# Optimization experiments

Hardware: AMD Instinct MI355X
Metric: run time of the kernel (lower is better)

Reference implementation:

```python
import jax, jax.numpy as jnp
import numpy as np

EPS = 1e-8  # matches torch F.cosine_similarity default eps


def setup_inputs() -> dict:
    key = jax.random.key(0)
    k1, k2, k3 = jax.random.split(key, 3)
    B, S, Q, T, D = 1, 5, 512, 64, 2048
    supp = jax.random.normal(k1, (B, S, T, D), dtype=jnp.float32)
    query = jax.random.normal(k2, (B, Q, T, D), dtype=jnp.float32)
    query_ys = jax.random.randint(k3, (Q,), 0, S, dtype=jnp.int64)
    return {"supp": supp, "query": query, "query_ys": query_ys}


def reference(supp, query, query_ys):
    # supp: [B, S, T, D], query: [B, Q, T, D]
    # Pool once over T (mathematically identical to repeat-then-mean).
    sp = supp.mean(axis=-2)   # [B, S, D]
    qp = query.mean(axis=-2)  # [B, Q, D]
    # Pairwise cosine similarity over D -> [B, Q, S]
    num = jnp.einsum('bqd,bsd->bqs', qp, sp)
    qn = jnp.linalg.norm(qp, axis=-1)  # [B, Q]
    sn = jnp.linalg.norm(sp, axis=-1)  # [B, S]
    denom = jnp.maximum(qn[:, :, None] * sn[:, None, :], EPS)
    dist = (num / denom)[0]  # squeeze(0) -> [Q, S]
    # Cross-entropy over the num_supp (class) axis
    logp = jax.nn.log_softmax(dist, axis=-1)
    loss = -jnp.take_along_axis(logp, query_ys[:, None], axis=1).mean()
    return (loss, 1.0 - dist)
```

## Files before the change

### kernel.cpp

```cpp
#include <hip/hip_runtime.h>
#include <hip/hip_bf16.h>

#define S_DIM 5
#define Q_DIM 512
#define T_DIM 64
#define D_DIM 2048
#define EPS_CS 1e-8f

typedef float f32x4 __attribute__((ext_vector_type(4)));

#define WS_SP     0
#define WS_SNPART 10240
#define WS_LOSS   10280
#define WS_CNT    10281

__device__ __forceinline__ float wave_reduce_sum(float v) {
    #pragma unroll
    for (int off = 32; off > 0; off >>= 1)
        v += __shfl_down(v, off, 64);
    return v;
}

__device__ __forceinline__ float dot4(f32x4 a, f32x4 b) {
    return a.x * b.x + a.y * b.y + a.z * b.z + a.w * b.w;
}

__global__ __launch_bounds__(512) void supp_pool_kernel(
    const float* __restrict__ supp, float* __restrict__ sp,
    float* __restrict__ snpart, float* __restrict__ loss_acc,
    unsigned int* __restrict__ counter)
{
    if (blockIdx.x == 0 && threadIdx.x == 0) {
        *loss_acc = 0.0f;
        *counter  = 0u;
    }

    const int s    = blockIdx.x >> 3;
    const int c    = blockIdx.x & 7;
    const int tg   = threadIdx.x >> 6;
    const int lane = threadIdx.x & 63;
    const int slot = c * 64 + lane;

    const f32x4* base = (const f32x4*)(supp + (size_t)s * T_DIM * D_DIM);

    f32x4 acc = {0.f, 0.f, 0.f, 0.f};
    #pragma unroll
    for (int i = 0; i < 8; ++i) {
        const int t = tg * 8 + i;
        acc += base[t * (D_DIM / 4) + slot];
    }

    __shared__ f32x4 lds[8][64];
    lds[tg][lane] = acc;
    __syncthreads();
    if (tg == 0) {
        f32x4 tot = lds[0][lane];
        #pragma unroll
        for (int w = 1; w < 8; ++w) tot += lds[w][lane];
        tot *= (1.0f / (float)T_DIM);
        ((f32x4*)(sp + (size_t)s * D_DIM))[slot] = tot;

        float sq = wave_reduce_sum(dot4(tot, tot));
        if (lane == 0) snpart[s * 8 + c] = sq;
    }
}

__global__ __launch_bounds__(512) void query_fused_kernel(
    const float* __restrict__ query, const float* __restrict__ sp,
    const float* __restrict__ snpart, const int* __restrict__ ys,
    float* __restrict__ out, float* __restrict__ loss_acc,
    unsigned int* __restrict__ counter)
{
    const int q   = blockIdx.x;
    const int tid = threadIdx.x;
    const f32x4* base = (const f32x4*)(query + (size_t)q * T_DIM * D_DIM);

    f32x4 acc = {0.f, 0.f, 0.f, 0.f};
    #pragma unroll 8
    for (int t = 0; t < T_DIM; ++t)
        acc += base[t * (D_DIM / 4) + tid];
    acc *= (1.0f / (float)T_DIM);

    float vals[6];
    vals[5] = dot4(acc, acc);
    #pragma unroll
    for (int s = 0; s < S_DIM; ++s) {
        f32x4 sv = ((const f32x4*)(sp + (size_t)s * D_DIM))[tid];
        vals[s] = dot4(acc, sv);
    }

    __shared__ float lds[8][6];
    const int wave = tid >> 6, lane = tid & 63;
    #pragma unroll
    for (int k = 0; k < 6; ++k) {
        float r = wave_reduce_sum(vals[k]);
        if (lane == 0) lds[wave][k] = r;
    }
    __syncthreads();

    if (tid == 0) {
        float tot[6];
        #pragma unroll
        for (int k = 0; k < 6; ++k) {
            float t = 0.f;
            #pragma unroll
            for (int w = 0; w < 8; ++w) t += lds[w][k];
            tot[k] = t;
        }
        const float qn = sqrtf(tot[5]);

        float dist[S_DIM];
        #pragma unroll
        for (int s = 0; s < S_DIM; ++s) {
            float sn2 = 0.f;
            #pragma unroll
            for (int c = 0; c < 8; ++c) sn2 += snpart[s * 8 + c];
            const float sn = sqrtf(sn2);
            const float d  = tot[s] / fmaxf(qn * sn, EPS_CS);
            dist[s] = d;
            out[1 + (size_t)q * S_DIM + s] = 1.0f - d;
        }

        float m = dist[0];
        #pragma unroll
        for (int s = 1; s < S_DIM; ++s) m = fmaxf(m, dist[s]);
        float sum = 0.f;
        #pragma unroll
        for (int s = 0; s < S_DIM; ++s) sum += expf(dist[s] - m);
        const float lse = m + logf(sum);

        int y = ys[q];
        if (y < 0) y = 0;
        if (y >= S_DIM) y = S_DIM - 1;
        const float nll = lse - dist[y];

        float oldv = atomicAdd(loss_acc, nll);
        __asm__ __volatile__("" :: "v"(oldv) : "memory");

        unsigned int old = atomicAdd(counter, 1u);
        if (old == Q_DIM - 1) {
            float tot_loss = atomicAdd(loss_acc, 0.0f);
            out[0] = tot_loss * (1.0f / (float)Q_DIM);
        }
    }
}

extern "C" void kernel_launch(void* const* d_in, const int* in_sizes, int n_in,
                              void* d_out, int out_size, void* d_ws, size_t ws_size,
                              hipStream_t stream) {
    const float* supp  = (const float*)d_in[0];
    const float* query = (const float*)d_in[1];
    const int*   ys    = (const int*)d_in[2];
    float* out = (float*)d_out;

    float* ws           = (float*)d_ws;
    float* sp           = ws + WS_SP;
    float* snpart       = ws + WS_SNPART;
    float* loss_acc     = ws + WS_LOSS;
    unsigned int* cnt   = (unsigned int*)(ws + WS_CNT);

    supp_pool_kernel<<<S_DIM * 8, 512, 0, stream>>>(supp, sp, snpart, loss_acc, cnt);
    query_fused_kernel<<<Q_DIM, 512, 0, stream>>>(query, sp, snpart, ys, out, loss_acc, cnt);
}
```

Baseline: 54.21 us.

## Split each query row across two blocks with atomic partial-dot combining

Each query is now handled by two blocks, each covering half of D, with two thread groups per block splitting the T reduction. Partial dot products and norms are accumulated with global atomics, and the second-arriving block finishes the cosine and loss computation. This aims to raise parallelism and memory-level concurrency for the bandwidth-bound pooling read. In exchange it adds per-query atomics and a workspace zeroing step.

Result: slower. 69.45 us (+28.1%).

```diff
diff --git a/kernel.cpp b/kernel.cpp
--- a/kernel.cpp
+++ b/kernel.cpp
@@ -9,10 +9,14 @@
 
 typedef float f32x4 __attribute__((ext_vector_type(4)));
 
-#define WS_SP     0
-#define WS_SNPART 10240
-#define WS_LOSS   10280
-#define WS_CNT    10281
+#define WS_SP      0
+#define WS_SNPART  10240
+#define WS_NUM     10280
+#define WS_QCNT    14376
+#define WS_LOSS    14888
+#define WS_LOSSCNT 14889
+#define WS_ZERO_BASE 10280
+#define WS_ZERO_LEN  4610
 
 __device__ __forceinline__ float wave_reduce_sum(float v) {
     #pragma unroll
@@ -26,14 +30,13 @@
 }
 
 __global__ __launch_bounds__(512) void supp_pool_kernel(
-    const float* __restrict__ supp, float* __restrict__ sp,
-    float* __restrict__ snpart, float* __restrict__ loss_acc,
-    unsigned int* __restrict__ counter)
+    const float* __restrict__ supp, float* __restrict__ ws)
 {
-    if (blockIdx.x == 0 && threadIdx.x == 0) {
-        *loss_acc = 0.0f;
-        *counter  = 0u;
-    }
+    float* sp     = ws + WS_SP;
+    float* snpart = ws + WS_SNPART;
+
+    const int gid = blockIdx.x * 512 + threadIdx.x;
+    if (gid < WS_ZERO_LEN) ws[WS_ZERO_BASE + gid] = 0.0f;
 
     const int s    = blockIdx.x >> 3;
     const int c    = blockIdx.x & 7;
@@ -65,82 +68,114 @@
     }
 }
 
-__global__ __launch_bounds__(512) void query_fused_kernel(
-    const float* __restrict__ query, const float* __restrict__ sp,
-    const float* __restrict__ snpart, const int* __restrict__ ys,
-    float* __restrict__ out, float* __restrict__ loss_acc,
-    unsigned int* __restrict__ counter)
+__global__ __launch_bounds__(512, 8) void query_fused_kernel(
+    const float* __restrict__ query, const int* __restrict__ ys,
+    float* __restrict__ out, float* __restrict__ ws)
 {
-    const int q   = blockIdx.x;
-    const int tid = threadIdx.x;
-    const f32x4* base = (const f32x4*)(query + (size_t)q * T_DIM * D_DIM);
+    const float* sp     = ws + WS_SP;
+    const float* snpart = ws + WS_SNPART;
+    float* num          = ws + WS_NUM;
+    unsigned int* qcnt  = (unsigned int*)(ws + WS_QCNT);
+    float* loss_acc     = ws + WS_LOSS;
+    unsigned int* lcnt  = (unsigned int*)(ws + WS_LOSSCNT);
+
+    const int q    = blockIdx.x >> 1;
+    const int h    = blockIdx.x & 1;
+    const int tid  = threadIdx.x;
+    const int tg   = tid >> 8;
+    const int sIdx = tid & 255;
+    const int slot = h * 256 + sIdx;
+
+    const f32x4* base = (const f32x4*)(query + (size_t)q * T_DIM * D_DIM) + slot;
 
     f32x4 acc = {0.f, 0.f, 0.f, 0.f};
-    #pragma unroll 8
-    for (int t = 0; t < T_DIM; ++t)
-        acc += base[t * (D_DIM / 4) + tid];
-    acc *= (1.0f / (float)T_DIM);
+    const int t0 = tg * 32;
+    #pragma unroll 4
+    for (int t = t0; t < t0 + 32; ++t)
+        acc += base[(size_t)t * (D_DIM / 4)];
 
-    float vals[6];
-    vals[5] = dot4(acc, acc);
-    #pragma unroll
-    for (int s = 0; s < S_DIM; ++s) {
-        f32x4 sv = ((const f32x4*)(sp + (size_t)s * D_DIM))[tid];
-        vals[s] = dot4(acc, sv);
-    }
+    __shared__ f32x4 comb[256];
+    __shared__ float lds2[4][6];
+    if (tg == 1) comb[sIdx] = acc;
+    __syncthreads();
 
-    __shared__ float lds[8][6];
-    const int wave = tid >> 6, lane = tid & 63;
-    #pragma unroll
-    for (int k = 0; k < 6; ++k) {
-        float r = wave_reduce_sum(vals[k]);
-        if (lane == 0) lds[wave][k] = r;
+    if (tg == 0) {
+        acc = (acc + comb[sIdx]) * (1.0f / (float)T_DIM);
+
+        float vals[6];
+        vals[5] = dot4(acc, acc);
+        #pragma unroll
+        for (int s = 0; s < S_DIM; ++s) {
+            f32x4 sv = ((const f32x4*)(sp + (size_t)s * D_DIM))[slot];
+            vals[s] = dot4(acc, sv);
+        }
+
+        const int wave = tid >> 6;
+        const int lane = tid & 63;
+        #pragma unroll
+        for (int k = 0; k < 6; ++k) {
+            float r = wave_reduce_sum(vals[k]);
+            if (lane == 0) lds2[wave][k] = r;
+        }
     }
     __syncthreads();
 
     if (tid == 0) {
-        float tot[6];
+        float part[6], olds[6];
         #pragma unroll
         for (int k = 0; k < 6; ++k) {
             float t = 0.f;
             #pragma unroll
-            for (int w = 0; w < 8; ++w) t += lds[w][k];
-            tot[k] = t;
+            for (int w = 0; w < 4; ++w) t += lds2[w][k];
+            part[k] = t;
+            olds[k] = atomicAdd(&num[(size_t)q * 8 + k], t);
         }
-        const float qn = sqrtf(tot[5]);
+        __asm__ __volatile__("" :: "v"(olds[0]), "v"(olds[1]), "v"(olds[2]),
+                                   "v"(olds[3]), "v"(olds[4]), "v"(olds[5])
+                                : "memory");
 
-        float dist[S_DIM];
-        #pragma unroll
-        for (int s = 0; s < S_DIM; ++s) {
-            float sn2 = 0.f;
+        unsigned int arrived = atomicAdd(&qcnt[q], 1u);
+        if (arrived == 1u) {
+            float tot[6];
             #pragma unroll
-            for (int c = 0; c < 8; ++c) sn2 += snpart[s * 8 + c];
-            const float sn = sqrtf(sn2);
-            const float d  = tot[s] / fmaxf(qn * sn, EPS_CS);
-            dist[s] = d;
-            out[1 + (size_t)q * S_DIM + s] = 1.0f - d;
-        }
+            for (int k = 0; k < 6; ++k)
+                tot[k] = atomicAdd(&num[(size_t)q * 8 + k], 0.0f);
 
-        float m = dist[0];
-        #pragma unroll
-        for (int s = 1; s < S_DIM; ++s) m = fmaxf(m, dist[s]);
-        float sum = 0.f;
-        #pragma unroll
-        for (int s = 0; s < S_DIM; ++s) sum += expf(dist[s] - m);
-        const float lse = m + logf(sum);
+            const float qn = sqrtf(tot[5]);
 
-        int y = ys[q];
-        if (y < 0) y = 0;
-        if (y >= S_DIM) y = S_DIM - 1;
-        const float nll = lse - dist[y];
+            float dist[S_DIM];
+            #pragma unroll
+            for (int s = 0; s < S_DIM; ++s) {
+                float sn2 = 0.f;
+                #pragma unroll
+                for (int c = 0; c < 8; ++c) sn2 += snpart[s * 8 + c];
+                const float sn = sqrtf(sn2);
+                const float d  = tot[s] / fmaxf(qn * sn, EPS_CS);
+                dist[s] = d;
+                out[1 + (size_t)q * S_DIM + s] = 1.0f - d;
+            }
 
-        float oldv = atomicAdd(loss_acc, nll);
-        __asm__ __volatile__("" :: "v"(oldv) : "memory");
+            float m = dist[0];
+            #pragma unroll
+            for (int s = 1; s < S_DIM; ++s) m = fmaxf(m, dist[s]);
+            float sum = 0.f;
+            #pragma unroll
+            for (int s = 0; s < S_DIM; ++s) sum += expf(dist[s] - m);
+            const float lse = m + logf(sum);
 
-        unsigned int old = atomicAdd(counter, 1u);
-        if (old == Q_DIM - 1) {
-            float tot_loss = atomicAdd(loss_acc, 0.0f);
-            out[0] = tot_loss * (1.0f / (float)Q_DIM);
+            int y = ys[q];
+            if (y < 0) y = 0;
+            if (y >= S_DIM) y = S_DIM - 1;
+            const float nll = lse - dist[y];
+
+            float oldl = atomicAdd(loss_acc, nll);
+            __asm__ __volatile__("" :: "v"(oldl) : "memory");
+
+            unsigned int done = atomicAdd(lcnt, 1u);
+            if (done == Q_DIM - 1) {
+                float tot_loss = atomicAdd(loss_acc, 0.0f);
+                out[0] = tot_loss * (1.0f / (float)Q_DIM);
+            }
         }
     }
 }
@@ -152,13 +187,8 @@
     const float* query = (const float*)d_in[1];
     const int*   ys    = (const int*)d_in[2];
     float* out = (float*)d_out;
+    float* ws  = (float*)d_ws;
 
-    float* ws           = (float*)d_ws;
-    float* sp           = ws + WS_SP;
-    float* snpart       = ws + WS_SNPART;
-    float* loss_acc     = ws + WS_LOSS;
-    unsigned int* cnt   = (unsigned int*)(ws + WS_CNT);
-
-    supp_pool_kernel<<<S_DIM * 8, 512, 0, stream>>>(supp, sp, snpart, loss_acc, cnt);
-    query_fused_kernel<<<Q_DIM, 512, 0, stream>>>(query, sp, snpart, ys, out, loss_acc, cnt);
+    supp_pool_kernel<<<S_DIM * 8, 512, 0, stream>>>(supp, ws);
+    query_fused_kernel<<<Q_DIM * 2, 512, 0, stream>>>(query, ys, out, ws);
 }
```
